# Optimization experiments

Measured on AMD Instinct MI355X. Metric: run time of the kernel, lower is better.

## Reference

```python
import jax, jax.numpy as jnp
import numpy as np

CHEB_K = 3
DIM_IN = 2
HIDDEN = 64
EMBED_DIM = 10
NODE_NUM = 2048
BATCH = 32


def _gconv(x, supports, W, b, cheb_k=CHEB_K):
    # Chebyshev graph conv applied directly to x (equivalent to building
    # T_k(A) matrices then applying: T_k(A) x = 2 A T_{k-1}(A) x - T_{k-2}(A) x).
    xs = [x, jnp.einsum('nm,bmc->bnc', supports, x)]
    for _ in range(2, cheb_k):
        xs.append(2.0 * jnp.einsum('nm,bmc->bnc', supports, xs[-1]) - xs[-2])
    x_g = jnp.concatenate(xs, axis=-1)          # [B, N, cheb_k*C]
    return jnp.einsum('bni,io->bno', x_g, W) + b


def setup_inputs() -> dict:
    key = jax.random.key(0)
    ks = jax.random.split(key, 7)
    c_in = DIM_IN + HIDDEN                       # 66
    # xavier_normal-ish scale for weights
    def xavier(k, fan_in, fan_out):
        std = float(np.sqrt(2.0 / (fan_in + fan_out)))
        return jax.random.normal(k, (fan_in, fan_out), dtype=jnp.float32) * std
    return {
        'x': jax.random.normal(ks[0], (BATCH, NODE_NUM, DIM_IN), dtype=jnp.float32),
        'state': jax.random.normal(ks[1], (BATCH, NODE_NUM, HIDDEN), dtype=jnp.float32),
        'node_embeddings': jax.random.normal(ks[2], (NODE_NUM, EMBED_DIM), dtype=jnp.float32),
        'W_gate': xavier(ks[3], CHEB_K * c_in, 2 * HIDDEN),
        'b_gate': jnp.zeros((2 * HIDDEN,), dtype=jnp.float32),
        'W_update': xavier(ks[4], CHEB_K * c_in, HIDDEN),
        'b_update': jnp.zeros((HIDDEN,), dtype=jnp.float32),
    }


def reference(x, state, node_embeddings, W_gate, b_gate, W_update, b_update):
    # adaptive adjacency: softmax(relu(E E^T), axis=1)
    logits = jnp.einsum('nc,mc->nm', node_embeddings, node_embeddings)
    supports = jax.nn.softmax(jax.nn.relu(logits), axis=1)   # [N, N]

    input_and_state = jnp.concatenate([x, state], axis=-1)   # [B, N, dim_in+hidden]
    z_r = jax.nn.sigmoid(_gconv(input_and_state, supports, W_gate, b_gate))
    z, r = jnp.split(z_r, 2, axis=-1)                        # each [B, N, hidden]
    candidate = jnp.concatenate([x, z * state], axis=-1)
    hc = jnp.tanh(_gconv(candidate, supports, W_update, b_update))
    h = r * state + (1.0 - r) * hc
    return h
```

## Files before the change

### kernel.cpp

```cpp
#include <hip/hip_runtime.h>


typedef __bf16 bf16x8 __attribute__((ext_vector_type(8)));
typedef __bf16 bf16x4 __attribute__((ext_vector_type(4)));
typedef float  f32x4  __attribute__((ext_vector_type(4)));

#define GLB(p) ((__attribute__((address_space(1))) void*)(void*)(p))
#define LDS(p) ((__attribute__((address_space(3))) void*)(p))

__global__ void prologue_kernel(const float* __restrict__ E, __bf16* __restrict__ S,
                                const float* __restrict__ Wg, __bf16* __restrict__ WTg,
                                const float* __restrict__ Wu, __bf16* __restrict__ WTu) {
    const int bid = blockIdx.x;
    const int t = threadIdx.x;
    __shared__ float sm[4], ss[4];
    if (bid >= 2048) {
        const float* W = (bid < 2176) ? Wg : Wu;
        __bf16* WT = (bid < 2176) ? WTg : WTu;
        const int Nout = (bid < 2176) ? 128 : 64;
        const int id = (bid - ((bid < 2176) ? 2048 : 2176)) * 256 + t;
        const int o = id >> 8, k = id & 255;
        const int jj = (k >= 144) ? 2 : (k >= 72 ? 1 : 0);
        const int cc = k - 72 * jj;
        const bool ok = (o < Nout) && (cc < 66) && (k < 216);
        WT[id] = ok ? (__bf16)W[(size_t)(66 * jj + cc) * Nout + o] : (__bf16)0.f;
        return;
    }
    const int n = bid;
    const int l = t & 63, w = t >> 6;
    float en[10];
#pragma unroll
    for (int i = 0; i < 10; ++i) en[i] = E[n * 10 + i];
    float vals[8];
    float mx = 0.f;
#pragma unroll
    for (int q = 0; q < 8; ++q) {
        const int m = q * 256 + t;
        const float* em = E + (size_t)m * 10;
        float d = 0.f;
#pragma unroll
        for (int i = 0; i < 10; ++i) d += en[i] * em[i];
        d = fmaxf(d, 0.f);
        vals[q] = d;
        mx = fmaxf(mx, d);
    }
#pragma unroll
    for (int off = 32; off; off >>= 1) mx = fmaxf(mx, __shfl_xor(mx, off));
    if (l == 0) sm[w] = mx;
    __syncthreads();
    mx = fmaxf(fmaxf(sm[0], sm[1]), fmaxf(sm[2], sm[3]));
    float sum = 0.f;
#pragma unroll
    for (int q = 0; q < 8; ++q) { vals[q] = __expf(vals[q] - mx); sum += vals[q]; }
#pragma unroll
    for (int off = 32; off; off >>= 1) sum += __shfl_xor(sum, off);
    if (l == 0) ss[w] = sum;
    __syncthreads();
    sum = ss[0] + ss[1] + ss[2] + ss[3];
    const float inv = 1.f / sum;
#pragma unroll
    for (int q = 0; q < 8; ++q) S[(size_t)n * 2048 + q * 256 + t] = (__bf16)(vals[q] * inv);
}

__global__ __launch_bounds__(256, 2)
void build_t2(const float* __restrict__ x, const float* __restrict__ st,
              const __bf16* __restrict__ zr, __bf16* __restrict__ T,
              __bf16* __restrict__ G) {
    __shared__ float Ls[66 * 129];
    const int b  = blockIdx.x >> 4;
    const int n0 = (blockIdx.x & 15) << 7;
    const int t = threadIdx.x;
    const size_t mb = (size_t)b * 2048 + n0;
    if (t < 128) {
        const float2 v = *(const float2*)&x[(mb + t) * 2];
        Ls[t] = v.x;
        Ls[129 + t] = v.y;
    }
#pragma unroll
    for (int r = 0; r < 8; ++r) {
        const int task = r * 256 + t;
        const int q = task & 15, n = task >> 4;
        f32x4 v = *(const f32x4*)&st[(mb + n) * 64 + q * 4];
        if (zr) {
            const bf16x4 z = *(const bf16x4*)&zr[(mb + n) * 128 + q * 4];
#pragma unroll
            for (int j = 0; j < 4; ++j) v[j] *= (float)z[j];
        }
        const int base = (2 + q * 4) * 129 + n;
#pragma unroll
        for (int j = 0; j < 4; ++j) Ls[base + j * 129] = v[j];
    }
    __syncthreads();
#pragma unroll
    for (int r = 0; r < 5; ++r) {
        const int task = r * 256 + t;
        if (task < 1056) {
            const int c = task >> 4, seg = task & 15;
            const float* src = &Ls[c * 129 + seg * 8];
            bf16x8 o;
#pragma unroll
            for (int j = 0; j < 8; ++j) o[j] = (__bf16)src[j];
            *(bf16x8*)&T[(size_t)(b * 66 + c) * 2048 + n0 + seg * 8] = o;
        }
    }
    {
        const int n = t & 127, half = t >> 7;
        const size_t grow = ((size_t)(b * 2048 + n0 + n)) * 256;
        for (int oct = half * 5; oct < (half ? 9 : 5); ++oct) {
            bf16x8 o8;
#pragma unroll
            for (int j = 0; j < 8; ++j) {
                const int cc = oct * 8 + j;
                o8[j] = (cc < 66) ? (__bf16)Ls[cc * 129 + n] : (__bf16)0.f;
            }
            *(bf16x8*)&G[grow + oct * 8] = o8;
        }
    }
}

__global__ __launch_bounds__(256, 3)
void gemm_pipe(const __bf16* __restrict__ A, int lda,
               const __bf16* __restrict__ Bt, int ldb,
               int K, int epi, int swz,
               __bf16* __restrict__ outT, const __bf16* __restrict__ subT,
               float* __restrict__ outF, const float* __restrict__ bias,
               __bf16* __restrict__ zrO, const __bf16* __restrict__ zrI,
               const float* __restrict__ state,
               __bf16* __restrict__ Gout, int gsec) {
    __shared__ __align__(16) __bf16 As[2][128 * 64];
    __shared__ __align__(16) __bf16 Bs[2][64 * 64];
    int mt, ct;
    if (swz) { mt = blockIdx.x & 15; ct = blockIdx.x >> 4; }
    else     { mt = blockIdx.x;      ct = blockIdx.y; }
    const int m0 = mt * 128, c0 = ct * 64;
    const int t = threadIdx.x;
    const int l = t & 63, w = t >> 6;
    const int wr = w >> 1, wc = w & 1;
    const int lm = l & 15, kq = l >> 4, lm7 = lm & 7;
    const int sr = l >> 3;
    const int gsw = (l & 7) ^ sr;

    f32x4 acc[4][2];
#pragma unroll
    for (int i = 0; i < 4; ++i)
#pragma unroll
        for (int j = 0; j < 2; ++j) acc[i][j] = (f32x4)0.f;

    const __bf16* Asrc = A  + (size_t)(m0 + w * 8 + sr) * lda + gsw * 8;
    const __bf16* Bsrc = Bt + (size_t)(c0 + w * 8 + sr) * ldb + gsw * 8;
    const int dstA = w * 512 + l * 8;

    auto stage = [&](int buf, int k0) {
#pragma unroll
        for (int q = 0; q < 4; ++q)
            __builtin_amdgcn_global_load_lds(GLB(Asrc + (size_t)q * 32 * lda + k0),
                                             LDS(&As[buf][q * 2048 + dstA]), 16, 0, 0);
#pragma unroll
        for (int q = 0; q < 2; ++q)
            __builtin_amdgcn_global_load_lds(GLB(Bsrc + (size_t)q * 32 * ldb + k0),
                                             LDS(&Bs[buf][q * 2048 + dstA]), 16, 0, 0);
    };
    auto compute = [&](int buf) {
        const __bf16* Ab = &As[buf][0];
        const __bf16* Bb = &Bs[buf][0];
#pragma unroll
        for (int ks = 0; ks < 2; ++ks) {
            const int ga = (((ks << 2) | kq) ^ lm7) << 3;
            bf16x8 af[4], bfr[2];
#pragma unroll
            for (int i = 0; i < 4; ++i)
                af[i] = *(const bf16x8*)&Ab[(wr * 64 + i * 16 + lm) * 64 + ga];
#pragma unroll
            for (int j = 0; j < 2; ++j)
                bfr[j] = *(const bf16x8*)&Bb[(wc * 32 + j * 16 + lm) * 64 + ga];
#pragma unroll
            for (int i = 0; i < 4; ++i)
#pragma unroll
                for (int j = 0; j < 2; ++j)
                    acc[i][j] = __builtin_amdgcn_mfma_f32_16x16x32_bf16(af[i], bfr[j], acc[i][j], 0, 0, 0);
        }
    };

    stage(0, 0);
    const int iters = K >> 6;
    for (int i = 0; i + 2 <= iters; i += 2) {
        stage(1, (i + 1) << 6);
        __builtin_amdgcn_sched_barrier(0);
        __builtin_amdgcn_s_waitcnt(0x0F76);
        __builtin_amdgcn_s_barrier();
        __builtin_amdgcn_sched_barrier(0);
        compute(0);
        __builtin_amdgcn_sched_barrier(0);
        __builtin_amdgcn_s_barrier();
        __builtin_amdgcn_sched_barrier(0);
        if (i + 2 < iters) {
            stage(0, (i + 2) << 6);
            __builtin_amdgcn_sched_barrier(0);
            __builtin_amdgcn_s_waitcnt(0x0F76);
        } else {
            __builtin_amdgcn_s_waitcnt(0x0F70);
        }
        __builtin_amdgcn_s_barrier();
        __builtin_amdgcn_sched_barrier(0);
        compute(1);
        __builtin_amdgcn_sched_barrier(0);
        if (i + 4 <= iters) {
            __builtin_amdgcn_s_barrier();
            __builtin_amdgcn_sched_barrier(0);
        }
    }

    const int rb0 = m0 + wr * 64 + kq * 4;
    const int cb0 = c0 + wc * 32 + lm;
#pragma unroll
    for (int i = 0; i < 4; ++i) {
        const int rbase = rb0 + i * 16;
#pragma unroll
        for (int j = 0; j < 2; ++j) {
            const int c = cb0 + j * 16;
            f32x4 v = acc[i][j];
            if (epi <= 1) {
                bf16x4 pk;
                if (epi == 0) {
#pragma unroll
                    for (int r = 0; r < 4; ++r) pk[r] = (__bf16)v[r];
                    *(bf16x4*)&outT[(size_t)c * 2048 + rbase] = pk;
                } else {
                    bf16x4 s = *(const bf16x4*)&subT[(size_t)c * 2048 + rbase];
#pragma unroll
                    for (int r = 0; r < 4; ++r) pk[r] = (__bf16)(2.f * v[r] - (float)s[r]);
                }
                const int b = c / 66, cc = c - b * 66;
                const size_t gb = ((size_t)(b * 2048 + rbase)) * 256 + gsec + cc;
#pragma unroll
                for (int r = 0; r < 4; ++r) Gout[gb + (size_t)r * 256] = pk[r];
            } else if (epi == 2) {
                const float bb = bias[c];
#pragma unroll
                for (int r = 0; r < 4; ++r) {
                    float xx = fminf(fmaxf(v[r] + bb, -30.f), 30.f);
                    zrO[(size_t)(rbase + r) * 128 + c] = (__bf16)(1.f / (1.f + __expf(-xx)));
                }
            } else {
                if (c < 64) {
                    const float bb = bias[c];
#pragma unroll
                    for (int r = 0; r < 4; ++r) {
                        const int m = rbase + r;
                        float xx = fminf(fmaxf(v[r] + bb, -15.f), 15.f);
                        float e = __expf(2.f * xx);
                        float hc = (e - 1.f) / (e + 1.f);
                        float rr = (float)zrI[(size_t)m * 128 + 64 + c];
                        float s = state[(size_t)m * 64 + c];
                        outF[(size_t)m * 64 + c] = rr * s + (1.f - rr) * hc;
                    }
                }
            }
        }
    }
}

extern "C" void kernel_launch(void* const* d_in, const int* in_sizes, int n_in,
                              void* d_out, int out_size, void* d_ws, size_t ws_size,
                              hipStream_t stream) {
    (void)in_sizes; (void)n_in; (void)out_size; (void)ws_size;
    const float* x  = (const float*)d_in[0];
    const float* st = (const float*)d_in[1];
    const float* E  = (const float*)d_in[2];
    const float* Wg = (const float*)d_in[3];
    const float* bg = (const float*)d_in[4];
    const float* Wu = (const float*)d_in[5];
    const float* bu = (const float*)d_in[6];
    float* out = (float*)d_out;

    char* p = (char*)d_ws;
    __bf16* S   = (__bf16*)p; p += (size_t)2048 * 2048 * 2;
    __bf16* T0  = (__bf16*)p; p += (size_t)2112 * 2048 * 2;
    __bf16* T1  = (__bf16*)p; p += (size_t)2112 * 2048 * 2;
    __bf16* G   = (__bf16*)p; p += (size_t)65536 * 256 * 2;
    __bf16* ZR  = (__bf16*)p; p += (size_t)65536 * 128 * 2;
    __bf16* WTg = (__bf16*)p; p += 128 * 256 * 2;
    __bf16* WTu = (__bf16*)p; p += 128 * 256 * 2;

    prologue_kernel<<<2304, 256, 0, stream>>>(E, S, Wg, WTg, Wu, WTu);

    build_t2<<<512, 256, 0, stream>>>(x, st, nullptr, T0, G);
    gemm_pipe<<<528, 256, 0, stream>>>(S, 2048, T0, 2048, 2048, 0, 1, T1, nullptr, nullptr, nullptr, nullptr, nullptr, nullptr, G, 72);
    gemm_pipe<<<528, 256, 0, stream>>>(S, 2048, T1, 2048, 2048, 1, 1, nullptr, T0, nullptr, nullptr, nullptr, nullptr, nullptr, G, 144);
    gemm_pipe<<<dim3(512, 2), 256, 0, stream>>>(G, 256, WTg, 256, 256, 2, 0, nullptr, nullptr, nullptr, bg, ZR, nullptr, nullptr, nullptr, 0);

    build_t2<<<512, 256, 0, stream>>>(x, st, ZR, T0, G);
    gemm_pipe<<<528, 256, 0, stream>>>(S, 2048, T0, 2048, 2048, 0, 1, T1, nullptr, nullptr, nullptr, nullptr, nullptr, nullptr, G, 72);
    gemm_pipe<<<528, 256, 0, stream>>>(S, 2048, T1, 2048, 2048, 1, 1, nullptr, T0, nullptr, nullptr, nullptr, nullptr, nullptr, G, 144);
    gemm_pipe<<<dim3(512, 1), 256, 0, stream>>>(G, 256, WTu, 256, 256, 3, 0, nullptr, nullptr, out, bu, nullptr, ZR, st, nullptr, 0);
}
```

Baseline: 264.6 us.

## Fold Chebyshev subtraction into weights and fuse build_t2 into prologue and gate epilogue

```diff
diff --git a/kernel.cpp b/kernel.cpp
--- a/kernel.cpp
+++ b/kernel.cpp
@@ -8,12 +8,62 @@
 #define GLB(p) ((__attribute__((address_space(1))) void*)(void*)(p))
 #define LDS(p) ((__attribute__((address_space(3))) void*)(p))
 
-__global__ void prologue_kernel(const float* __restrict__ E, __bf16* __restrict__ S,
-                                const float* __restrict__ Wg, __bf16* __restrict__ WTg,
-                                const float* __restrict__ Wu, __bf16* __restrict__ WTu) {
+__global__ __launch_bounds__(256, 2)
+void prologue_kernel(const float* __restrict__ E, __bf16* __restrict__ S,
+                     const float* __restrict__ Wg, __bf16* __restrict__ WTg,
+                     const float* __restrict__ Wu, __bf16* __restrict__ WTu,
+                     const float* __restrict__ x, const float* __restrict__ st,
+                     __bf16* __restrict__ T, __bf16* __restrict__ G) {
     const int bid = blockIdx.x;
     const int t = threadIdx.x;
-    __shared__ float sm[4], ss[4];
+    __shared__ float Ls[66 * 129];
+    if (bid >= 2304) {
+        const int rb = bid - 2304;
+        const int b  = rb >> 4;
+        const int n0 = (rb & 15) << 7;
+        const size_t mb = (size_t)b * 2048 + n0;
+        if (t < 128) {
+            const float2 v = *(const float2*)&x[(mb + t) * 2];
+            Ls[t] = v.x;
+            Ls[129 + t] = v.y;
+        }
+#pragma unroll
+        for (int r = 0; r < 8; ++r) {
+            const int task = r * 256 + t;
+            const int q = task & 15, n = task >> 4;
+            f32x4 v = *(const f32x4*)&st[(mb + n) * 64 + q * 4];
+            const int base = (2 + q * 4) * 129 + n;
+#pragma unroll
+            for (int j = 0; j < 4; ++j) Ls[base + j * 129] = v[j];
+        }
+        __syncthreads();
+#pragma unroll
+        for (int r = 0; r < 5; ++r) {
+            const int task = r * 256 + t;
+            if (task < 1056) {
+                const int c = task >> 4, seg = task & 15;
+                const float* src = &Ls[c * 129 + seg * 8];
+                bf16x8 o;
+#pragma unroll
+                for (int j = 0; j < 8; ++j) o[j] = (__bf16)src[j];
+                *(bf16x8*)&T[(size_t)(b * 66 + c) * 2048 + n0 + seg * 8] = o;
+            }
+        }
+        {
+            const int n = t & 127, half = t >> 7;
+            const size_t grow = ((size_t)(b * 2048 + n0 + n)) * 256;
+            for (int oct = half * 5; oct < (half ? 9 : 5); ++oct) {
+                bf16x8 o8;
+#pragma unroll
+                for (int j = 0; j < 8; ++j) {
+                    const int cc = oct * 8 + j;
+                    o8[j] = (cc < 66) ? (__bf16)Ls[cc * 129 + n] : (__bf16)0.f;
+                }
+                *(bf16x8*)&G[grow + oct * 8] = o8;
+            }
+        }
+        return;
+    }
     if (bid >= 2048) {
         const float* W = (bid < 2176) ? Wg : Wu;
         __bf16* WT = (bid < 2176) ? WTg : WTu;
@@ -23,11 +73,19 @@
         const int jj = (k >= 144) ? 2 : (k >= 72 ? 1 : 0);
         const int cc = k - 72 * jj;
         const bool ok = (o < Nout) && (cc < 66) && (k < 216);
-        WT[id] = ok ? (__bf16)W[(size_t)(66 * jj + cc) * Nout + o] : (__bf16)0.f;
+        float v = 0.f;
+        if (ok) {
+            if (jj == 0)      v = W[(size_t)cc * Nout + o] - W[(size_t)(132 + cc) * Nout + o];
+            else if (jj == 1) v = W[(size_t)(66 + cc) * Nout + o];
+            else              v = 2.f * W[(size_t)(132 + cc) * Nout + o];
+        }
+        WT[id] = (__bf16)v;
         return;
     }
     const int n = bid;
     const int l = t & 63, w = t >> 6;
+    float* sm = Ls;
+    float* ss = Ls + 4;
     float en[10];
 #pragma unroll
     for (int i = 0; i < 10; ++i) en[i] = E[n * 10 + i];
@@ -60,62 +118,6 @@
     const float inv = 1.f / sum;
 #pragma unroll
     for (int q = 0; q < 8; ++q) S[(size_t)n * 2048 + q * 256 + t] = (__bf16)(vals[q] * inv);
-}
-
-__global__ __launch_bounds__(256, 2)
-void build_t2(const float* __restrict__ x, const float* __restrict__ st,
-              const __bf16* __restrict__ zr, __bf16* __restrict__ T,
-              __bf16* __restrict__ G) {
-    __shared__ float Ls[66 * 129];
-    const int b  = blockIdx.x >> 4;
-    const int n0 = (blockIdx.x & 15) << 7;
-    const int t = threadIdx.x;
-    const size_t mb = (size_t)b * 2048 + n0;
-    if (t < 128) {
-        const float2 v = *(const float2*)&x[(mb + t) * 2];
-        Ls[t] = v.x;
-        Ls[129 + t] = v.y;
-    }
-#pragma unroll
-    for (int r = 0; r < 8; ++r) {
-        const int task = r * 256 + t;
-        const int q = task & 15, n = task >> 4;
-        f32x4 v = *(const f32x4*)&st[(mb + n) * 64 + q * 4];
-        if (zr) {
-            const bf16x4 z = *(const bf16x4*)&zr[(mb + n) * 128 + q * 4];
-#pragma unroll
-            for (int j = 0; j < 4; ++j) v[j] *= (float)z[j];
-        }
-        const int base = (2 + q * 4) * 129 + n;
-#pragma unroll
-        for (int j = 0; j < 4; ++j) Ls[base + j * 129] = v[j];
-    }
-    __syncthreads();
-#pragma unroll
-    for (int r = 0; r < 5; ++r) {
-        const int task = r * 256 + t;
-        if (task < 1056) {
-            const int c = task >> 4, seg = task & 15;
-            const float* src = &Ls[c * 129 + seg * 8];
-            bf16x8 o;
-#pragma unroll
-            for (int j = 0; j < 8; ++j) o[j] = (__bf16)src[j];
-            *(bf16x8*)&T[(size_t)(b * 66 + c) * 2048 + n0 + seg * 8] = o;
-        }
-    }
-    {
-        const int n = t & 127, half = t >> 7;
-        const size_t grow = ((size_t)(b * 2048 + n0 + n)) * 256;
-        for (int oct = half * 5; oct < (half ? 9 : 5); ++oct) {
-            bf16x8 o8;
-#pragma unroll
-            for (int j = 0; j < 8; ++j) {
-                const int cc = oct * 8 + j;
-                o8[j] = (cc < 66) ? (__bf16)Ls[cc * 129 + n] : (__bf16)0.f;
-            }
-            *(bf16x8*)&G[grow + oct * 8] = o8;
-        }
-    }
 }
 
 __global__ __launch_bounds__(256, 3)
@@ -126,7 +128,8 @@
                float* __restrict__ outF, const float* __restrict__ bias,
                __bf16* __restrict__ zrO, const __bf16* __restrict__ zrI,
                const float* __restrict__ state,
-               __bf16* __restrict__ Gout, int gsec) {
+               __bf16* __restrict__ Gout, int gsec,
+               const float* __restrict__ xin) {
     __shared__ __align__(16) __bf16 As[2][128 * 64];
     __shared__ __align__(16) __bf16 Bs[2][64 * 64];
     int mt, ct;
@@ -221,25 +224,34 @@
             f32x4 v = acc[i][j];
             if (epi <= 1) {
                 bf16x4 pk;
-                if (epi == 0) {
-#pragma unroll
-                    for (int r = 0; r < 4; ++r) pk[r] = (__bf16)v[r];
+#pragma unroll
+                for (int r = 0; r < 4; ++r) pk[r] = (__bf16)v[r];
+                if (epi == 0)
                     *(bf16x4*)&outT[(size_t)c * 2048 + rbase] = pk;
-                } else {
-                    bf16x4 s = *(const bf16x4*)&subT[(size_t)c * 2048 + rbase];
-#pragma unroll
-                    for (int r = 0; r < 4; ++r) pk[r] = (__bf16)(2.f * v[r] - (float)s[r]);
-                }
                 const int b = c / 66, cc = c - b * 66;
                 const size_t gb = ((size_t)(b * 2048 + rbase)) * 256 + gsec + cc;
 #pragma unroll
                 for (int r = 0; r < 4; ++r) Gout[gb + (size_t)r * 256] = pk[r];
             } else if (epi == 2) {
                 const float bb = bias[c];
-#pragma unroll
-                for (int r = 0; r < 4; ++r) {
-                    float xx = fminf(fmaxf(v[r] + bb, -30.f), 30.f);
-                    zrO[(size_t)(rbase + r) * 128 + c] = (__bf16)(1.f / (1.f + __expf(-xx)));
+                if (c < 64) {
+                    const int b = rbase >> 11, n = rbase & 2047;
+                    bf16x4 pk;
+#pragma unroll
+                    for (int r = 0; r < 4; ++r) {
+                        float xx = fminf(fmaxf(v[r] + bb, -30.f), 30.f);
+                        const float z = 1.f / (1.f + __expf(-xx));
+                        const float sv = state[(size_t)(rbase + r) * 64 + c];
+                        pk[r] = (__bf16)(z * sv);
+                        Gout[((size_t)(rbase + r)) * 256 + 2 + c] = pk[r];
+                    }
+                    *(bf16x4*)&outT[(size_t)(b * 66 + 2 + c) * 2048 + n] = pk;
+                } else {
+#pragma unroll
+                    for (int r = 0; r < 4; ++r) {
+                        float xx = fminf(fmaxf(v[r] + bb, -30.f), 30.f);
+                        zrO[(size_t)(rbase + r) * 64 + (c - 64)] = (__bf16)(1.f / (1.f + __expf(-xx)));
+                    }
                 }
             } else {
                 if (c < 64) {
@@ -250,13 +262,24 @@
                         float xx = fminf(fmaxf(v[r] + bb, -15.f), 15.f);
                         float e = __expf(2.f * xx);
                         float hc = (e - 1.f) / (e + 1.f);
-                        float rr = (float)zrI[(size_t)m * 128 + 64 + c];
+                        float rr = (float)zrI[(size_t)m * 64 + c];
                         float s = state[(size_t)m * 64 + c];
                         outF[(size_t)m * 64 + c] = rr * s + (1.f - rr) * hc;
                     }
                 }
             }
         }
+    }
+    if (epi == 2 && c0 == 0 && t < 128) {
+        const int m = m0 + t;
+        const int b = m >> 11, n = m & 2047;
+        const float2 vx = *(const float2*)&xin[(size_t)m * 2];
+        outT[(size_t)(b * 66) * 2048 + n]     = (__bf16)vx.x;
+        outT[(size_t)(b * 66 + 1) * 2048 + n] = (__bf16)vx.y;
+        Gout[(size_t)m * 256 + 0] = (__bf16)vx.x;
+        Gout[(size_t)m * 256 + 1] = (__bf16)vx.y;
+#pragma unroll
+        for (int cc = 66; cc < 72; ++cc) Gout[(size_t)m * 256 + cc] = (__bf16)0.f;
     }
 }
 
@@ -277,20 +300,19 @@
     __bf16* S   = (__bf16*)p; p += (size_t)2048 * 2048 * 2;
     __bf16* T0  = (__bf16*)p; p += (size_t)2112 * 2048 * 2;
     __bf16* T1  = (__bf16*)p; p += (size_t)2112 * 2048 * 2;
-    __bf16* G   = (__bf16*)p; p += (size_t)65536 * 256 * 2;
-    __bf16* ZR  = (__bf16*)p; p += (size_t)65536 * 128 * 2;
+    __bf16* Gg  = (__bf16*)p; p += (size_t)65536 * 256 * 2;
+    __bf16* Gu  = (__bf16*)p; p += (size_t)65536 * 256 * 2;
+    __bf16* ZR  = (__bf16*)p; p += (size_t)65536 * 64 * 2;
     __bf16* WTg = (__bf16*)p; p += 128 * 256 * 2;
     __bf16* WTu = (__bf16*)p; p += 128 * 256 * 2;
 
-    prologue_kernel<<<2304, 256, 0, stream>>>(E, S, Wg, WTg, Wu, WTu);
-
-    build_t2<<<512, 256, 0, stream>>>(x, st, nullptr, T0, G);
-    gemm_pipe<<<528, 256, 0, stream>>>(S, 2048, T0, 2048, 2048, 0, 1, T1, nullptr, nullptr, nullptr, nullptr, nullptr, nullptr, G, 72);
-    gemm_pipe<<<528, 256, 0, stream>>>(S, 2048, T1, 2048, 2048, 1, 1, nullptr, T0, nullptr, nullptr, nullptr, nullptr, nullptr, G, 144);
-    gemm_pipe<<<dim3(512, 2), 256, 0, stream>>>(G, 256, WTg, 256, 256, 2, 0, nullptr, nullptr, nullptr, bg, ZR, nullptr, nullptr, nullptr, 0);
-
-    build_t2<<<512, 256, 0, stream>>>(x, st, ZR, T0, G);
-    gemm_pipe<<<528, 256, 0, stream>>>(S, 2048, T0, 2048, 2048, 0, 1, T1, nullptr, nullptr, nullptr, nullptr, nullptr, nullptr, G, 72);
-    gemm_pipe<<<528, 256, 0, stream>>>(S, 2048, T1, 2048, 2048, 1, 1, nullptr, T0, nullptr, nullptr, nullptr, nullptr, nullptr, G, 144);
-    gemm_pipe<<<dim3(512, 1), 256, 0, stream>>>(G, 256, WTu, 256, 256, 3, 0, nullptr, nullptr, out, bu, nullptr, ZR, st, nullptr, 0);
+    prologue_kernel<<<2816, 256, 0, stream>>>(E, S, Wg, WTg, Wu, WTu, x, st, T0, Gg);
+
+    gemm_pipe<<<528, 256, 0, stream>>>(S, 2048, T0, 2048, 2048, 0, 1, T1, nullptr, nullptr, nullptr, nullptr, nullptr, nullptr, Gg, 72, nullptr);
+    gemm_pipe<<<528, 256, 0, stream>>>(S, 2048, T1, 2048, 2048, 1, 1, nullptr, nullptr, nullptr, nullptr, nullptr, nullptr, nullptr, Gg, 144, nullptr);
+    gemm_pipe<<<dim3(512, 2), 256, 0, stream>>>(Gg, 256, WTg, 256, 256, 2, 0, T0, nullptr, nullptr, bg, ZR, nullptr, st, Gu, 0, x);
+
+    gemm_pipe<<<528, 256, 0, stream>>>(S, 2048, T0, 2048, 2048, 0, 1, T1, nullptr, nullptr, nullptr, nullptr, nullptr, nullptr, Gu, 72, nullptr);
+    gemm_pipe<<<528, 256, 0, stream>>>(S, 2048, T1, 2048, 2048, 1, 1, nullptr, nullptr, nullptr, nullptr, nullptr, nullptr, nullptr, Gu, 144, nullptr);
+    gemm_pipe<<<dim3(512, 1), 256, 0, stream>>>(Gu, 256, WTu, 256, 256, 3, 0, nullptr, nullptr, out, bu, nullptr, ZR, st, nullptr, 0, nullptr);
 }
```

New measurement: 258.6 us. 1.02x faster.
